# Kernel tuning notes

Measured on AMD Instinct MI355X. Metric: run time of the kernel, lower is better.

The kernel has to match this reference:

```python
import jax, jax.numpy as jnp
import numpy as np

B, N, M, C, KV, H = 2, 1024, 2048, 1024, 768, 16
D = C // H
SCALE = D ** -0.5  # qk_scale defaults to head_dim**-0.5


def setup_inputs() -> dict:
    key = jax.random.key(0)
    ks = jax.random.split(key, 8)
    return {
        "q": jax.random.normal(ks[0], (B, N, C), jnp.float32),
        "kv": jax.random.normal(ks[1], (B, M, KV), jnp.float32),
        "alibi_bias": jax.random.normal(ks[2], (B, H, N, M), jnp.float32) * 0.02,
        "padding_mask": jax.random.randint(ks[3], (B, M), 0, 2).astype(bool),
        "Wq": jax.random.normal(ks[4], (C, C), jnp.float32) * 0.02,
        "Wkv": jax.random.normal(ks[5], (2 * C, KV), jnp.float32) * 0.02,
        "Wproj": jax.random.normal(ks[6], (C, C), jnp.float32) * 0.02,
        "bproj": jnp.zeros((C,), jnp.float32),
    }


def reference(q, kv, alibi_bias, Wq, Wkv, Wproj, bproj, padding_mask):
    Bq, Nq, Cq = q.shape
    # q projection -> (B, H, N, D)
    qh = (q @ Wq.T).reshape(Bq, Nq, H, D).transpose(0, 2, 1, 3)
    # kv projection -> (2, B, H, M, D)
    kvp = (kv @ Wkv.T).reshape(Bq, -1, 2, H, D).transpose(2, 0, 3, 1, 4)
    k, v = kvp[0], kvp[1]
    # scaled dot-product scores (B, H, N, M)
    attn = jnp.einsum('bhnd,bhmd->bhnm', qh * SCALE, k)
    attn = attn + alibi_bias
    attn = jnp.where(padding_mask[:, None, None, :], -jnp.inf, attn)
    # softmax in fp32, cast back to q dtype (matches torch softmax(dtype=float32))
    attn = jax.nn.softmax(attn.astype(jnp.float32), axis=-1).astype(q.dtype)
    x = jnp.einsum('bhnm,bhmd->bhnd', attn, v).transpose(0, 2, 1, 3).reshape(Bq, Nq, Cq)
    return x @ Wproj.T + bproj
```

## Files before the change

### kernel.cpp

```cpp
#include <hip/hip_runtime.h>
#include <hip/hip_bf16.h>
#include <hip/hip_fp16.h>

#define B_  2
#define N_  1024
#define M_  2048
#define C_  1024
#define KV_ 768
#define H_  16
#define D_  64

typedef _Float16 half8 __attribute__((ext_vector_type(8)));
typedef float f32x4 __attribute__((ext_vector_type(4)));

template<int MD, int ND, int KD, int EPI>
__global__ __launch_bounds__(256)
void gemm_bt(const float* __restrict__ A, const float* __restrict__ Bm,
             void* __restrict__ out0, void* __restrict__ out1,
             const float* __restrict__ bias)
{
    __shared__ _Float16 As[128][40];
    __shared__ _Float16 Bs[128][40];

    const int tid  = threadIdx.x;
    const int lane = tid & 63;
    const int w    = tid >> 6;
    const int l16  = lane & 15;
    const int quad = lane >> 4;
    const int wm   = w >> 1, wn = w & 1;
    const int m0   = blockIdx.y * 128;
    const int n0   = blockIdx.x * 128;

    f32x4 acc[4][4];
    {
        f32x4 z = {0.f, 0.f, 0.f, 0.f};
        for (int i = 0; i < 4; i++) for (int j = 0; j < 4; j++) acc[i][j] = z;
    }

    for (int k0 = 0; k0 < KD; k0 += 32) {
        __syncthreads();
        #pragma unroll
        for (int i = 0; i < 4; i++) {
            int idx = tid + 256 * i;
            int row = idx >> 3, c4 = idx & 7;
            float4 v = *(const float4*)(A + (size_t)(m0 + row) * KD + k0 + c4 * 4);
            union { _Float16 h[4]; uint2 u; } pk;
            pk.h[0] = (_Float16)v.x; pk.h[1] = (_Float16)v.y;
            pk.h[2] = (_Float16)v.z; pk.h[3] = (_Float16)v.w;
            *(uint2*)&As[row][c4 * 4] = pk.u;
        }
        #pragma unroll
        for (int i = 0; i < 4; i++) {
            int idx = tid + 256 * i;
            int row = idx >> 3, c4 = idx & 7;
            float4 v = *(const float4*)(Bm + (size_t)(n0 + row) * KD + k0 + c4 * 4);
            union { _Float16 h[4]; uint2 u; } pk;
            pk.h[0] = (_Float16)v.x; pk.h[1] = (_Float16)v.y;
            pk.h[2] = (_Float16)v.z; pk.h[3] = (_Float16)v.w;
            *(uint2*)&Bs[row][c4 * 4] = pk.u;
        }
        __syncthreads();

        half8 af[4], bf[4];
        #pragma unroll
        for (int i = 0; i < 4; i++) af[i] = *(const half8*)&As[wm * 64 + i * 16 + l16][quad * 8];
        #pragma unroll
        for (int j = 0; j < 4; j++) bf[j] = *(const half8*)&Bs[wn * 64 + j * 16 + l16][quad * 8];
        #pragma unroll
        for (int i = 0; i < 4; i++)
            #pragma unroll
            for (int j = 0; j < 4; j++)
                acc[i][j] = __builtin_amdgcn_mfma_f32_16x16x32_f16(af[i], bf[j], acc[i][j], 0, 0, 0);
    }

    #pragma unroll
    for (int i = 0; i < 4; i++)
        #pragma unroll
        for (int j = 0; j < 4; j++)
            #pragma unroll
            for (int r = 0; r < 4; r++) {
                int m = m0 + wm * 64 + i * 16 + quad * 4 + r;
                int n = n0 + wn * 64 + j * 16 + l16;
                float v = acc[i][j][r];
                if (EPI == 0) {
                    ((_Float16*)out0)[(size_t)m * ND + n] = (_Float16)(v * 0.125f);
                } else if (EPI == 1) {
                    int b = m >> 11, ml = m & 2047;
                    if (n < C_) {
                        int h = n >> 6, d = n & 63;
                        ((_Float16*)out0)[((size_t)(b * H_ + h) * M_ + ml) * D_ + d] = (_Float16)v;
                    } else {
                        int h = (n >> 6) & 15, d = n & 63;
                        ((_Float16*)out1)[((size_t)(b * H_ + h) * D_ + d) * M_ + ml] = (_Float16)v;
                    }
                } else {
                    ((float*)out0)[(size_t)m * ND + n] = v + bias[n];
                }
            }
}

__global__ __launch_bounds__(256)
void flash_attn(const _Float16* __restrict__ qw, const _Float16* __restrict__ kw,
                const _Float16* __restrict__ vw, const float* __restrict__ alibi,
                const void* __restrict__ pmask, float* __restrict__ xw)
{
    __shared__ _Float16 Ks[64][72];
    __shared__ _Float16 Vs[64][72];
    __shared__ _Float16 Ps[4][16][72];
    __shared__ int mflag;

    const int tid  = threadIdx.x;
    const int lane = tid & 63;
    const int w    = tid >> 6;
    const int l16  = lane & 15;
    const int quad = lane >> 4;
    const int nt   = blockIdx.x;
    const int bh   = blockIdx.y;
    const int b    = bh >> 4;
    const int h    = bh & 15;
    const int n0   = nt * 64;

    if (tid == 0) {
        const unsigned int* p32 = (const unsigned int*)pmask;
        unsigned int a = 0;
        for (int i = 0; i < 64; i++) a |= p32[i] & 0xFFFFFF00u;
        mflag = (a == 0) ? 1 : 0;
    }
    __syncthreads();
    const int mi = mflag;

    half8 qf[2];
    {
        const _Float16* qp = qw + ((size_t)(b * N_ + n0 + w * 16 + l16) * C_) + h * 64 + quad * 8;
        qf[0] = *(const half8*)qp;
        qf[1] = *(const half8*)(qp + 32);
    }

    f32x4 accO[4];
    float mrow[4], lrow[4];
    {
        f32x4 z = {0.f, 0.f, 0.f, 0.f};
        for (int i = 0; i < 4; i++) accO[i] = z;
    }
    #pragma unroll
    for (int r = 0; r < 4; r++) { mrow[r] = -1e30f; lrow[r] = 0.f; }

    const _Float16* kbase = kw + (size_t)bh * (M_ * D_);
    const _Float16* vbase = vw + (size_t)bh * (D_ * M_);
    const float*    abase = alibi + (size_t)bh * ((size_t)N_ * M_) + (size_t)n0 * M_;
    const unsigned char* pm8  = (const unsigned char*)pmask;
    const int*           pm32 = (const int*)pmask;

    for (int m0 = 0; m0 < M_; m0 += 64) {
        __syncthreads();
        #pragma unroll
        for (int i = 0; i < 2; i++) {
            int idx = tid + 256 * i;
            int row = idx >> 3, seg = idx & 7;
            *(uint4*)&Ks[row][seg * 8] = *(const uint4*)(kbase + (size_t)(m0 + row) * D_ + seg * 8);
            *(uint4*)&Vs[row][seg * 8] = *(const uint4*)(vbase + (size_t)row * M_ + m0 + seg * 8);
        }
        __syncthreads();

        f32x4 s[4];
        {
            f32x4 z = {0.f, 0.f, 0.f, 0.f};
            for (int j = 0; j < 4; j++) s[j] = z;
        }
        #pragma unroll
        for (int j = 0; j < 4; j++) {
            half8 kf0 = *(const half8*)&Ks[j * 16 + l16][quad * 8];
            half8 kf1 = *(const half8*)&Ks[j * 16 + l16][32 + quad * 8];
            s[j] = __builtin_amdgcn_mfma_f32_16x16x32_f16(qf[0], kf0, s[j], 0, 0, 0);
            s[j] = __builtin_amdgcn_mfma_f32_16x16x32_f16(qf[1], kf1, s[j], 0, 0, 0);
        }

        #pragma unroll
        for (int j = 0; j < 4; j++) {
            int mcol = m0 + j * 16 + l16;
            int msk;
            if (mi) msk = pm32[b * M_ + mcol];
            else    msk = (int)pm8[b * M_ + mcol];
            const float* ap = abase + (size_t)(w * 16 + quad * 4) * M_ + mcol;
            #pragma unroll
            for (int r = 0; r < 4; r++) {
                float sv = s[j][r] + ap[(size_t)r * M_];
                s[j][r] = msk ? -1e30f : sv;
            }
        }

        float mx[4];
        #pragma unroll
        for (int r = 0; r < 4; r++)
            mx[r] = fmaxf(fmaxf(s[0][r], s[1][r]), fmaxf(s[2][r], s[3][r]));
        #pragma unroll
        for (int off = 1; off < 16; off <<= 1)
            #pragma unroll
            for (int r = 0; r < 4; r++) mx[r] = fmaxf(mx[r], __shfl_xor(mx[r], off, 64));

        float alpha[4], rs[4];
        #pragma unroll
        for (int r = 0; r < 4; r++) {
            float mn = fmaxf(mrow[r], mx[r]);
            alpha[r] = exp2f((mrow[r] - mn) * 1.44269504f);
            mrow[r] = mn;
            rs[r] = 0.f;
        }
        #pragma unroll
        for (int j = 0; j < 4; j++)
            #pragma unroll
            for (int r = 0; r < 4; r++) {
                float p = exp2f((s[j][r] - mrow[r]) * 1.44269504f);
                s[j][r] = p;
                rs[r] += p;
            }
        #pragma unroll
        for (int off = 1; off < 16; off <<= 1)
            #pragma unroll
            for (int r = 0; r < 4; r++) rs[r] += __shfl_xor(rs[r], off, 64);
        #pragma unroll
        for (int r = 0; r < 4; r++) lrow[r] = lrow[r] * alpha[r] + rs[r];

        #pragma unroll
        for (int j = 0; j < 4; j++)
            #pragma unroll
            for (int r = 0; r < 4; r++)
                Ps[w][quad * 4 + r][j * 16 + l16] = (_Float16)s[j][r];

        #pragma unroll
        for (int dt = 0; dt < 4; dt++)
            #pragma unroll
            for (int r = 0; r < 4; r++) accO[dt][r] *= alpha[r];
        #pragma unroll
        for (int kk = 0; kk < 2; kk++) {
            half8 pf = *(const half8*)&Ps[w][l16][kk * 32 + quad * 8];
            #pragma unroll
            for (int dt = 0; dt < 4; dt++) {
                half8 vf = *(const half8*)&Vs[dt * 16 + l16][kk * 32 + quad * 8];
                accO[dt] = __builtin_amdgcn_mfma_f32_16x16x32_f16(pf, vf, accO[dt], 0, 0, 0);
            }
        }
    }

    #pragma unroll
    for (int dt = 0; dt < 4; dt++)
        #pragma unroll
        for (int r = 0; r < 4; r++) {
            int n = n0 + w * 16 + quad * 4 + r;
            xw[(size_t)(b * N_ + n) * C_ + h * 64 + dt * 16 + l16] = accO[dt][r] / lrow[r];
        }
}

extern "C" void kernel_launch(void* const* d_in, const int* in_sizes, int n_in,
                              void* d_out, int out_size, void* d_ws, size_t ws_size,
                              hipStream_t stream)
{
    const float* q     = (const float*)d_in[0];
    const float* kv    = (const float*)d_in[1];
    const float* alibi = (const float*)d_in[2];
    const void*  pmask = d_in[3];
    const float* Wq    = (const float*)d_in[4];
    const float* Wkv   = (const float*)d_in[5];
    const float* Wproj = (const float*)d_in[6];
    const float* bproj = (const float*)d_in[7];
    float* out = (float*)d_out;

    char* ws = (char*)d_ws;
    _Float16* q_ws = (_Float16*)ws;
    _Float16* k_ws = (_Float16*)(ws + (4u  << 20));
    _Float16* v_ws = (_Float16*)(ws + (12u << 20));
    float*    x_ws = (float*)   (ws + (20u << 20));

    gemm_bt<B_*N_, C_, C_, 0><<<dim3(C_/128, (B_*N_)/128), 256, 0, stream>>>(
        q, Wq, (void*)q_ws, nullptr, nullptr);
    gemm_bt<B_*M_, 2*C_, KV_, 1><<<dim3((2*C_)/128, (B_*M_)/128), 256, 0, stream>>>(
        kv, Wkv, (void*)k_ws, (void*)v_ws, nullptr);
    flash_attn<<<dim3(N_/64, B_*H_), 256, 0, stream>>>(q_ws, k_ws, v_ws, alibi, pmask, x_ws);
    gemm_bt<B_*N_, C_, C_, 2><<<dim3(C_/128, (B_*N_)/128), 256, 0, stream>>>(
        x_ws, Wproj, (void*)out, nullptr, bproj);
}
```

Baseline: 560.3 us.

## Pre-convert inputs to fp16, use LDS-direct loads in GEMMs, widen attention tile

Adds separate fp32-to-fp16 conversion kernels for activations and weights, folding the q scale into the q conversion. The GEMMs now take fp16 inputs and fill a swizzled LDS layout with global_load_lds. The attention kernel processes 128 keys per iteration instead of 64, computes the mask-type flag with a ballot, and writes its output as fp16 for the final projection. This cuts fp32 traffic and conversion work inside the GEMM loops, at the cost of extra kernel launches and more LDS per attention block.

```diff
diff --git a/kernel.cpp b/kernel.cpp
--- a/kernel.cpp
+++ b/kernel.cpp
@@ -13,14 +13,35 @@
 typedef _Float16 half8 __attribute__((ext_vector_type(8)));
 typedef float f32x4 __attribute__((ext_vector_type(4)));
 
-template<int MD, int ND, int KD, int EPI>
+__device__ inline void gload16(const _Float16* g, _Float16* l) {
+    __builtin_amdgcn_global_load_lds(
+        (const __attribute__((address_space(1))) unsigned int*)g,
+        (__attribute__((address_space(3))) unsigned int*)l, 16, 0, 0);
+}
+
 __global__ __launch_bounds__(256)
-void gemm_bt(const float* __restrict__ A, const float* __restrict__ Bm,
-             void* __restrict__ out0, void* __restrict__ out1,
-             const float* __restrict__ bias)
+void f32tof16(const float* __restrict__ s, _Float16* __restrict__ d, int n4, float scale)
 {
-    __shared__ _Float16 As[128][40];
-    __shared__ _Float16 Bs[128][40];
+    int i = blockIdx.x * 256 + threadIdx.x;
+    if (i < n4) {
+        float4 v = ((const float4*)s)[i];
+        union { _Float16 h[4]; unsigned long long u; } pk;
+        pk.h[0] = (_Float16)(v.x * scale);
+        pk.h[1] = (_Float16)(v.y * scale);
+        pk.h[2] = (_Float16)(v.z * scale);
+        pk.h[3] = (_Float16)(v.w * scale);
+        ((unsigned long long*)d)[i] = pk.u;
+    }
+}
+
+template<int ND, int KD, int EPI>
+__global__ __launch_bounds__(256)
+void gemm16(const _Float16* __restrict__ A, const _Float16* __restrict__ Bm,
+            void* __restrict__ out0, void* __restrict__ out1,
+            const float* __restrict__ bias)
+{
+    __shared__ _Float16 As[128 * 32];
+    __shared__ _Float16 Bs[128 * 32];
 
     const int tid  = threadIdx.x;
     const int lane = tid & 63;
@@ -31,6 +52,10 @@
     const int m0   = blockIdx.y * 128;
     const int n0   = blockIdx.x * 128;
 
+    const int srow = tid >> 2;
+    const int scol = ((tid & 3) ^ (srow & 3)) * 8;
+    const int ldso = srow * 32 + (tid & 3) * 8;
+
     f32x4 acc[4][4];
     {
         f32x4 z = {0.f, 0.f, 0.f, 0.f};
@@ -39,33 +64,23 @@
 
     for (int k0 = 0; k0 < KD; k0 += 32) {
         __syncthreads();
+        gload16(A  + (size_t)(m0 + srow)      * KD + k0 + scol, As + ldso);
+        gload16(A  + (size_t)(m0 + 64 + srow) * KD + k0 + scol, As + 64 * 32 + ldso);
+        gload16(Bm + (size_t)(n0 + srow)      * KD + k0 + scol, Bs + ldso);
+        gload16(Bm + (size_t)(n0 + 64 + srow) * KD + k0 + scol, Bs + 64 * 32 + ldso);
+        __syncthreads();
+
+        half8 af[4], bf[4];
         #pragma unroll
         for (int i = 0; i < 4; i++) {
-            int idx = tid + 256 * i;
-            int row = idx >> 3, c4 = idx & 7;
-            float4 v = *(const float4*)(A + (size_t)(m0 + row) * KD + k0 + c4 * 4);
-            union { _Float16 h[4]; uint2 u; } pk;
-            pk.h[0] = (_Float16)v.x; pk.h[1] = (_Float16)v.y;
-            pk.h[2] = (_Float16)v.z; pk.h[3] = (_Float16)v.w;
-            *(uint2*)&As[row][c4 * 4] = pk.u;
-        }
-        #pragma unroll
-        for (int i = 0; i < 4; i++) {
-            int idx = tid + 256 * i;
-            int row = idx >> 3, c4 = idx & 7;
-            float4 v = *(const float4*)(Bm + (size_t)(n0 + row) * KD + k0 + c4 * 4);
-            union { _Float16 h[4]; uint2 u; } pk;
-            pk.h[0] = (_Float16)v.x; pk.h[1] = (_Float16)v.y;
-            pk.h[2] = (_Float16)v.z; pk.h[3] = (_Float16)v.w;
-            *(uint2*)&Bs[row][c4 * 4] = pk.u;
-        }
-        __syncthreads();
-
-        half8 af[4], bf[4];
-        #pragma unroll
-        for (int i = 0; i < 4; i++) af[i] = *(const half8*)&As[wm * 64 + i * 16 + l16][quad * 8];
-        #pragma unroll
-        for (int j = 0; j < 4; j++) bf[j] = *(const half8*)&Bs[wn * 64 + j * 16 + l16][quad * 8];
+            int r = wm * 64 + i * 16 + l16;
+            af[i] = *(const half8*)&As[r * 32 + ((quad ^ (r & 3)) * 8)];
+        }
+        #pragma unroll
+        for (int j = 0; j < 4; j++) {
+            int r = wn * 64 + j * 16 + l16;
+            bf[j] = *(const half8*)&Bs[r * 32 + ((quad ^ (r & 3)) * 8)];
+        }
         #pragma unroll
         for (int i = 0; i < 4; i++)
             #pragma unroll
@@ -83,7 +98,7 @@
                 int n = n0 + wn * 64 + j * 16 + l16;
                 float v = acc[i][j][r];
                 if (EPI == 0) {
-                    ((_Float16*)out0)[(size_t)m * ND + n] = (_Float16)(v * 0.125f);
+                    ((_Float16*)out0)[(size_t)m * ND + n] = (_Float16)v;
                 } else if (EPI == 1) {
                     int b = m >> 11, ml = m & 2047;
                     if (n < C_) {
@@ -102,11 +117,11 @@
 __global__ __launch_bounds__(256)
 void flash_attn(const _Float16* __restrict__ qw, const _Float16* __restrict__ kw,
                 const _Float16* __restrict__ vw, const float* __restrict__ alibi,
-                const void* __restrict__ pmask, float* __restrict__ xw)
+                const void* __restrict__ pmask, _Float16* __restrict__ xw)
 {
-    __shared__ _Float16 Ks[64][72];
-    __shared__ _Float16 Vs[64][72];
-    __shared__ _Float16 Ps[4][16][72];
+    __shared__ _Float16 Ks[128][72];
+    __shared__ _Float16 Vs[64][136];
+    __shared__ _Float16 Ps[4][16][136];
     __shared__ int mflag;
 
     const int tid  = threadIdx.x;
@@ -114,17 +129,15 @@
     const int w    = tid >> 6;
     const int l16  = lane & 15;
     const int quad = lane >> 4;
-    const int nt   = blockIdx.x;
     const int bh   = blockIdx.y;
     const int b    = bh >> 4;
     const int h    = bh & 15;
-    const int n0   = nt * 64;
-
-    if (tid == 0) {
-        const unsigned int* p32 = (const unsigned int*)pmask;
-        unsigned int a = 0;
-        for (int i = 0; i < 64; i++) a |= p32[i] & 0xFFFFFF00u;
-        mflag = (a == 0) ? 1 : 0;
+    const int n0   = blockIdx.x * 64;
+
+    if (tid < 64) {
+        unsigned a = ((const unsigned*)pmask)[tid] & 0xFFFFFF00u;
+        unsigned long long anyset = __ballot(a != 0);
+        if (tid == 0) mflag = (anyset == 0ull) ? 1 : 0;
     }
     __syncthreads();
     const int mi = mflag;
@@ -147,28 +160,30 @@
 
     const _Float16* kbase = kw + (size_t)bh * (M_ * D_);
     const _Float16* vbase = vw + (size_t)bh * (D_ * M_);
-    const float*    abase = alibi + (size_t)bh * ((size_t)N_ * M_) + (size_t)n0 * M_;
+    const float*    abase = alibi + (size_t)bh * ((size_t)N_ * M_) + (size_t)n0 * M_
+                          + (size_t)(w * 16 + quad * 4) * M_;
     const unsigned char* pm8  = (const unsigned char*)pmask;
     const int*           pm32 = (const int*)pmask;
 
-    for (int m0 = 0; m0 < M_; m0 += 64) {
+    for (int m0 = 0; m0 < M_; m0 += 128) {
         __syncthreads();
         #pragma unroll
-        for (int i = 0; i < 2; i++) {
-            int idx = tid + 256 * i;
-            int row = idx >> 3, seg = idx & 7;
-            *(uint4*)&Ks[row][seg * 8] = *(const uint4*)(kbase + (size_t)(m0 + row) * D_ + seg * 8);
-            *(uint4*)&Vs[row][seg * 8] = *(const uint4*)(vbase + (size_t)row * M_ + m0 + seg * 8);
+        for (int i = 0; i < 4; i++) {
+            int s = tid + 256 * i;
+            int kr = s >> 3, kc = s & 7;
+            *(uint4*)&Ks[kr][kc * 8] = *(const uint4*)(kbase + (size_t)(m0 + kr) * D_ + kc * 8);
+            int vr = s >> 4, vc = s & 15;
+            *(uint4*)&Vs[vr][vc * 8] = *(const uint4*)(vbase + (size_t)vr * M_ + m0 + vc * 8);
         }
         __syncthreads();
 
-        f32x4 s[4];
+        f32x4 s[8];
         {
             f32x4 z = {0.f, 0.f, 0.f, 0.f};
-            for (int j = 0; j < 4; j++) s[j] = z;
-        }
-        #pragma unroll
-        for (int j = 0; j < 4; j++) {
+            for (int j = 0; j < 8; j++) s[j] = z;
+        }
+        #pragma unroll
+        for (int j = 0; j < 8; j++) {
             half8 kf0 = *(const half8*)&Ks[j * 16 + l16][quad * 8];
             half8 kf1 = *(const half8*)&Ks[j * 16 + l16][32 + quad * 8];
             s[j] = __builtin_amdgcn_mfma_f32_16x16x32_f16(qf[0], kf0, s[j], 0, 0, 0);
@@ -176,12 +191,10 @@
         }
 
         #pragma unroll
-        for (int j = 0; j < 4; j++) {
+        for (int j = 0; j < 8; j++) {
             int mcol = m0 + j * 16 + l16;
-            int msk;
-            if (mi) msk = pm32[b * M_ + mcol];
-            else    msk = (int)pm8[b * M_ + mcol];
-            const float* ap = abase + (size_t)(w * 16 + quad * 4) * M_ + mcol;
+            int msk = mi ? pm32[b * M_ + mcol] : (int)pm8[b * M_ + mcol];
+            const float* ap = abase + mcol;
             #pragma unroll
             for (int r = 0; r < 4; r++) {
                 float sv = s[j][r] + ap[(size_t)r * M_];
@@ -191,8 +204,11 @@
 
         float mx[4];
         #pragma unroll
-        for (int r = 0; r < 4; r++)
-            mx[r] = fmaxf(fmaxf(s[0][r], s[1][r]), fmaxf(s[2][r], s[3][r]));
+        for (int r = 0; r < 4; r++) {
+            mx[r] = s[0][r];
+            #pragma unroll
+            for (int j = 1; j < 8; j++) mx[r] = fmaxf(mx[r], s[j][r]);
+        }
         #pragma unroll
         for (int off = 1; off < 16; off <<= 1)
             #pragma unroll
@@ -207,7 +223,7 @@
             rs[r] = 0.f;
         }
         #pragma unroll
-        for (int j = 0; j < 4; j++)
+        for (int j = 0; j < 8; j++)
             #pragma unroll
             for (int r = 0; r < 4; r++) {
                 float p = exp2f((s[j][r] - mrow[r]) * 1.44269504f);
@@ -222,7 +238,7 @@
         for (int r = 0; r < 4; r++) lrow[r] = lrow[r] * alpha[r] + rs[r];
 
         #pragma unroll
-        for (int j = 0; j < 4; j++)
+        for (int j = 0; j < 8; j++)
             #pragma unroll
             for (int r = 0; r < 4; r++)
                 Ps[w][quad * 4 + r][j * 16 + l16] = (_Float16)s[j][r];
@@ -231,8 +247,9 @@
         for (int dt = 0; dt < 4; dt++)
             #pragma unroll
             for (int r = 0; r < 4; r++) accO[dt][r] *= alpha[r];
-        #pragma unroll
-        for (int kk = 0; kk < 2; kk++) {
+
+        #pragma unroll
+        for (int kk = 0; kk < 4; kk++) {
             half8 pf = *(const half8*)&Ps[w][l16][kk * 32 + quad * 8];
             #pragma unroll
             for (int dt = 0; dt < 4; dt++) {
@@ -247,7 +264,8 @@
         #pragma unroll
         for (int r = 0; r < 4; r++) {
             int n = n0 + w * 16 + quad * 4 + r;
-            xw[(size_t)(b * N_ + n) * C_ + h * 64 + dt * 16 + l16] = accO[dt][r] / lrow[r];
+            xw[(size_t)(b * N_ + n) * C_ + h * 64 + dt * 16 + l16] =
+                (_Float16)(accO[dt][r] / lrow[r]);
         }
 }
 
@@ -265,17 +283,35 @@
     const float* bproj = (const float*)d_in[7];
     float* out = (float*)d_out;
 
+    const size_t MB = 1u << 20;
     char* ws = (char*)d_ws;
-    _Float16* q_ws = (_Float16*)ws;
-    _Float16* k_ws = (_Float16*)(ws + (4u  << 20));
-    _Float16* v_ws = (_Float16*)(ws + (12u << 20));
-    float*    x_ws = (float*)   (ws + (20u << 20));
-
-    gemm_bt<B_*N_, C_, C_, 0><<<dim3(C_/128, (B_*N_)/128), 256, 0, stream>>>(
-        q, Wq, (void*)q_ws, nullptr, nullptr);
-    gemm_bt<B_*M_, 2*C_, KV_, 1><<<dim3((2*C_)/128, (B_*M_)/128), 256, 0, stream>>>(
-        kv, Wkv, (void*)k_ws, (void*)v_ws, nullptr);
-    flash_attn<<<dim3(N_/64, B_*H_), 256, 0, stream>>>(q_ws, k_ws, v_ws, alibi, pmask, x_ws);
-    gemm_bt<B_*N_, C_, C_, 2><<<dim3(C_/128, (B_*N_)/128), 256, 0, stream>>>(
-        x_ws, Wproj, (void*)out, nullptr, bproj);
-}
+    _Float16* qh     = (_Float16*)(ws + 0 * MB);
+    _Float16* kvh    = (_Float16*)(ws + 4 * MB);
+    _Float16* Wqh    = (_Float16*)(ws + 12 * MB);
+    _Float16* Wkvh   = (_Float16*)(ws + 14 * MB);
+    _Float16* Wprojh = (_Float16*)(ws + 18 * MB);
+    _Float16* qp     = (_Float16*)(ws + 20 * MB);
+    _Float16* k_ws   = (_Float16*)(ws + 24 * MB);
+    _Float16* v_ws   = (_Float16*)(ws + 33 * MB);
+    _Float16* x_ws   = (_Float16*)(ws + 42 * MB);
+
+    const int nq  = B_ * N_ * C_ / 4;
+    const int nkv = B_ * M_ * KV_ / 4;
+    const int nwq = C_ * C_ / 4;
+    const int nwk = 2 * C_ * KV_ / 4;
+
+    f32tof16<<<(nq  + 255) / 256, 256, 0, stream>>>(q,     qh,     nq,  0.125f);
+    f32tof16<<<(nkv + 255) / 256, 256, 0, stream>>>(kv,    kvh,    nkv, 1.0f);
+    f32tof16<<<(nwq + 255) / 256, 256, 0, stream>>>(Wq,    Wqh,    nwq, 1.0f);
+    f32tof16<<<(nwk + 255) / 256, 256, 0, stream>>>(Wkv,   Wkvh,   nwk, 1.0f);
+    f32tof16<<<(nwq + 255) / 256, 256, 0, stream>>>(Wproj, Wprojh, nwq, 1.0f);
+
+    gemm16<C_, C_, 0><<<dim3(C_ / 128, (B_ * N_) / 128), 256, 0, stream>>>(
+        qh, Wqh, (void*)qp, nullptr, nullptr);
+    gemm16<2 * C_, KV_, 1><<<dim3((2 * C_) / 128, (B_ * M_) / 128), 256, 0, stream>>>(
+        kvh, Wkvh, (void*)k_ws, (void*)v_ws, nullptr);
+    flash_attn<<<dim3(N_ / 64, B_ * H_), 256, 0, stream>>>(
+        qp, k_ws, v_ws, alibi, pmask, x_ws);
+    gemm16<C_, C_, 2><<<dim3(C_ / 128, (B_ * N_) / 128), 256, 0, stream>>>(
+        x_ws, Wprojh, (void*)out, nullptr, bproj);
+}
```

After: 507.9 us. 1.1x faster.
